# Kernel tuning notes

Measured on AMD Instinct MI355X. Metric: run time of the kernel, lower is better.

The kernel has to match this reference:

```python
import jax, jax.numpy as jnp
import numpy as np

B, S, HID = 2, 2048, 4096
NH, NKV, HD = 32, 8, 128
SCALING = HD ** -0.5
Q_SIZE = NH * HD          # 4096
KV_SIZE = NKV * HD        # 1024
GROUPS = NH // NKV        # 4


def setup_inputs() -> dict:
    key = jax.random.key(0)
    ks = jax.random.split(key, 5)
    hidden_states = jax.random.normal(ks[0], (B, S, HID), dtype=jnp.float32)
    # Realistic rotary embeddings: cos/sin of position-dependent angles, HF layout [B, S, HD]
    inv_freq = 1.0 / (10000.0 ** (jnp.arange(0, HD, 2, dtype=jnp.float32) / HD))  # [HD/2]
    pos = jnp.arange(S, dtype=jnp.float32)
    freqs = pos[:, None] * inv_freq[None, :]                 # [S, HD/2]
    emb = jnp.concatenate([freqs, freqs], axis=-1)           # [S, HD]
    cos = jnp.broadcast_to(jnp.cos(emb), (B, S, HD))
    sin = jnp.broadcast_to(jnp.sin(emb), (B, S, HD))
    w_qkv = jax.random.normal(ks[1], (Q_SIZE + 2 * KV_SIZE, HID), dtype=jnp.float32) * (HID ** -0.5)
    w_o = jax.random.normal(ks[2], (HID, Q_SIZE), dtype=jnp.float32) * (Q_SIZE ** -0.5)
    return {"hidden_states": hidden_states, "cos": cos, "sin": sin, "w_qkv": w_qkv, "w_o": w_o}


def _rotate_half(x):
    x1, x2 = jnp.split(x, 2, axis=-1)
    return jnp.concatenate([-x2, x1], axis=-1)


def reference(hidden_states, cos, sin, w_qkv, w_o):
    b, s, _ = hidden_states.shape
    # Fused QKV projection (attention_bias=False for llama)
    qkv = jnp.einsum('bsh,oh->bso', hidden_states, w_qkv)    # [B, S, Q+2KV]
    q = qkv[..., :Q_SIZE].reshape(b, s, NH, HD).transpose(0, 2, 1, 3)                       # [B, NH, S, D]
    k = qkv[..., Q_SIZE:Q_SIZE + KV_SIZE].reshape(b, s, NKV, HD).transpose(0, 2, 1, 3)      # [B, NKV, S, D]
    v = qkv[..., Q_SIZE + KV_SIZE:].reshape(b, s, NKV, HD).transpose(0, 2, 1, 3)            # [B, NKV, S, D]
    # Rotary position embedding (HF apply_rotary_pos_emb, unsqueeze over heads)
    c = cos[:, None, :, :]
    sn = sin[:, None, :, :]
    q = q * c + _rotate_half(q) * sn
    k = k * c + _rotate_half(k) * sn
    # GQA: repeat KV heads across groups
    k = jnp.repeat(k, GROUPS, axis=1)   # [B, NH, S, D]
    v = jnp.repeat(v, GROUPS, axis=1)
    # Causal SDPA
    scores = jnp.einsum('bhqd,bhkd->bhqk', q, k) * SCALING
    causal = jnp.tril(jnp.ones((s, s), dtype=bool))
    scores = jnp.where(causal[None, None], scores, jnp.finfo(scores.dtype).min)
    attn = jax.nn.softmax(scores, axis=-1)
    out = jnp.einsum('bhqk,bhkd->bhqd', attn, v)             # [B, NH, S, D]
    out = out.transpose(0, 2, 1, 3).reshape(b, s, Q_SIZE)    # [B, S, HID]
    return jnp.einsum('bso,ho->bsh', out, w_o)
```

## Files before the change

### kernel.cpp

```cpp
#include <hip/hip_runtime.h>
#include <hip/hip_bf16.h>
#include <cstdint>

#define B_DIM 2
#define S_LEN 2048
#define HID 4096
#define NH 32
#define NKV 8
#define HD 128
#define QSZ (NH * HD)
#define KVSZ (NKV * HD)
#define QKVW (QSZ + 2 * KVSZ)
#define SCALING 0.08838834764831845f

typedef __bf16 bf16;
typedef __bf16 bf16x4 __attribute__((ext_vector_type(4)));
typedef __bf16 bf16x8 __attribute__((ext_vector_type(8)));
typedef float floatx4 __attribute__((ext_vector_type(4)));

typedef __attribute__((address_space(1))) void GV;
typedef __attribute__((address_space(3))) void SV;

#define BAR() __builtin_amdgcn_s_barrier()
#define SCHED_FENCE() __builtin_amdgcn_sched_barrier(0)

__global__ __launch_bounds__(256) void cvt2(const float* __restrict__ a, bf16* __restrict__ oa, int na4,
                                            const float* __restrict__ b, bf16* __restrict__ ob, int nb4) {
    int total = na4 + nb4;
    int stride = gridDim.x * blockDim.x;
    for (int i = blockIdx.x * blockDim.x + threadIdx.x; i < total; i += stride) {
        const float* src; bf16* dst; int j = i;
        if (j < na4) { src = a; dst = oa; }
        else { j -= na4; src = b; dst = ob; }
        float4 v = ((const float4*)src)[j];
        bf16x4 o;
        o[0] = (bf16)v.x; o[1] = (bf16)v.y; o[2] = (bf16)v.z; o[3] = (bf16)v.w;
        ((bf16x4*)dst)[j] = o;
    }
}

template <int MODE, typename OutT>
__global__ __launch_bounds__(512, 2) void gemm256(const bf16* __restrict__ A,
                                                  const bf16* __restrict__ Bm,
                                                  OutT* __restrict__ C,
                                                  bf16* __restrict__ Qo,
                                                  bf16* __restrict__ Ko,
                                                  bf16* __restrict__ Vo,
                                                  const float* __restrict__ cosp,
                                                  const float* __restrict__ sinp,
                                                  const float* __restrict__ cvt_src,
                                                  bf16* __restrict__ cvt_dst,
                                                  int cvt_n4, int ngemm,
                                                  int M, int N, int K) {
    __shared__ __align__(16) char smem[131072];
    (void)M;
    int bid = blockIdx.x;
    int tid = threadIdx.x;
    if (bid >= ngemm) {
        int stride = (gridDim.x - ngemm) * 512;
        for (int i = (bid - ngemm) * 512 + tid; i < cvt_n4; i += stride) {
            float4 v = ((const float4*)cvt_src)[i];
            bf16x4 o;
            o[0] = (bf16)v.x; o[1] = (bf16)v.y; o[2] = (bf16)v.z; o[3] = (bf16)v.w;
            ((bf16x4*)cvt_dst)[i] = o;
        }
        return;
    }
    int tiles_n = N >> 8;
    int wg = (bid & 7) * (ngemm >> 3) + (bid >> 3);
    int bm = wg / tiles_n, bn = wg % tiles_n;
    int lane = tid & 63, w = tid >> 6;
    int l15 = lane & 15, lg = lane >> 4, l7 = l15 & 7;
    int wm = w >> 2, wn = w & 3;
    const bf16* Ab = A + (size_t)bm * 256 * K;
    const bf16* Bb = Bm + (size_t)bn * 256 * K;

    auto AsP = [&](int buf, int h) -> char* { return smem + (buf * 2 + h) * 16384; };
    auto BsP = [&](int buf, int h) -> char* { return smem + 65536 + (buf * 2 + h) * 16384; };

    int o_lo = tid * 16, o_hi = o_lo + 8192;
    int r_lo = o_lo >> 7, r_hi = o_hi >> 7;
    int eo0 = r_lo * K + ((((o_lo >> 4) & 7) ^ (r_lo & 7)) << 3);
    int eo1 = r_hi * K + ((((o_hi >> 4) & 7) ^ (r_hi & 7)) << 3);
    const bf16* AbH[2] = {Ab, Ab + (size_t)128 * K};
    const bf16* BbH[2] = {Bb, Bb + (size_t)128 * K};

    auto stageA = [&](int buf, int h, int kt) {
        const bf16* base = AbH[h] + kt * 64;
        __builtin_amdgcn_global_load_lds((GV*)(base + eo0), (SV*)(AsP(buf, h) + o_lo), 16, 0, 0);
        __builtin_amdgcn_global_load_lds((GV*)(base + eo1), (SV*)(AsP(buf, h) + o_hi), 16, 0, 0);
    };
    auto stageB = [&](int buf, int h, int kt) {
        const bf16* base = BbH[h] + kt * 64;
        __builtin_amdgcn_global_load_lds((GV*)(base + eo0), (SV*)(BsP(buf, h) + o_lo), 16, 0, 0);
        __builtin_amdgcn_global_load_lds((GV*)(base + eo1), (SV*)(BsP(buf, h) + o_hi), 16, 0, 0);
    };
    auto rdA = [&](int buf, int fr, int kk) -> bf16x8 {
        int off = (fr * 16 + l15) * 128 + ((((kk << 2) | lg) ^ l7) << 4);
        return *(const bf16x8*)(AsP(buf, wm) + off);
    };
    auto rdB = [&](int buf, int fc, int kk) -> bf16x8 {
        int off = ((wn & 1) * 64 + fc * 16 + l15) * 128 + ((((kk << 2) | lg) ^ l7) << 4);
        return *(const bf16x8*)(BsP(buf, wn >> 1) + off);
    };

    floatx4 acc[8][4] = {};
    bf16x8 aF[4][2], bF[4][2];
    int nk = K >> 6, niter = nk >> 1;

    stageA(0, 0, 0); stageA(0, 1, 0); stageB(0, 0, 0); stageB(0, 1, 0);
    stageB(1, 0, 1); stageB(1, 1, 1);
    asm volatile("s_waitcnt vmcnt(4)" ::: "memory");
    SCHED_FENCE();
    BAR();

    auto quad = [&](int ra, int ca) {
        __builtin_amdgcn_s_setprio(1);
#pragma unroll
        for (int fr = 0; fr < 4; ++fr)
#pragma unroll
            for (int fc = 0; fc < 2; ++fc)
#pragma unroll
                for (int kk = 0; kk < 2; ++kk)
                    acc[ra * 4 + fr][ca * 2 + fc] = __builtin_amdgcn_mfma_f32_16x16x32_bf16(
                        aF[fr][kk], bF[ca * 2 + fc][kk], acc[ra * 4 + fr][ca * 2 + fc], 0, 0, 0);
        __builtin_amdgcn_s_setprio(0);
    };

    for (int i = 0; i < niter; ++i) {
        bool nl = (i + 1 < niter);
        int kt1 = 2 * i + 1, kt2 = 2 * i + 2, kt3 = 2 * i + 3;
#pragma unroll
        for (int fr = 0; fr < 4; ++fr)
#pragma unroll
            for (int kk = 0; kk < 2; ++kk) aF[fr][kk] = rdA(0, fr, kk);
#pragma unroll
        for (int fc = 0; fc < 2; ++fc)
#pragma unroll
            for (int kk = 0; kk < 2; ++kk) bF[fc][kk] = rdB(0, fc, kk);
        stageA(1, 0, kt1);
        BAR(); quad(0, 0); BAR();
#pragma unroll
        for (int fc = 2; fc < 4; ++fc)
#pragma unroll
            for (int kk = 0; kk < 2; ++kk) bF[fc][kk] = rdB(0, fc, kk);
        stageA(1, 1, kt1);
        BAR(); quad(0, 1); BAR();
#pragma unroll
        for (int fr = 0; fr < 4; ++fr)
#pragma unroll
            for (int kk = 0; kk < 2; ++kk) aF[fr][kk] = rdA(0, 4 + fr, kk);
        if (nl) stageB(0, 0, kt2);
        BAR(); quad(1, 0); BAR();
        if (nl) stageB(0, 1, kt2);
        BAR(); quad(1, 1);
        if (nl) asm volatile("s_waitcnt vmcnt(4)" ::: "memory");
        else    asm volatile("s_waitcnt vmcnt(0)" ::: "memory");
        SCHED_FENCE();
        BAR();
#pragma unroll
        for (int fr = 0; fr < 4; ++fr)
#pragma unroll
            for (int kk = 0; kk < 2; ++kk) aF[fr][kk] = rdA(1, fr, kk);
#pragma unroll
        for (int fc = 0; fc < 2; ++fc)
#pragma unroll
            for (int kk = 0; kk < 2; ++kk) bF[fc][kk] = rdB(1, fc, kk);
        if (nl) stageA(0, 0, kt2);
        BAR(); quad(0, 0); BAR();
#pragma unroll
        for (int fc = 2; fc < 4; ++fc)
#pragma unroll
            for (int kk = 0; kk < 2; ++kk) bF[fc][kk] = rdB(1, fc, kk);
        if (nl) stageA(0, 1, kt2);
        BAR(); quad(0, 1); BAR();
#pragma unroll
        for (int fr = 0; fr < 4; ++fr)
#pragma unroll
            for (int kk = 0; kk < 2; ++kk) aF[fr][kk] = rdA(1, 4 + fr, kk);
        if (nl) stageB(1, 0, kt3);
        BAR(); quad(1, 0); BAR();
        if (nl) stageB(1, 1, kt3);
        BAR(); quad(1, 1);
        asm volatile("s_waitcnt vmcnt(4)" ::: "memory");
        SCHED_FENCE();
        BAR();
    }

    if constexpr (MODE == 0) {
        int brow = bm * 256 + wm * 128, bcol = bn * 256 + wn * 64;
#pragma unroll
        for (int fr = 0; fr < 8; ++fr)
#pragma unroll
            for (int fc = 0; fc < 4; ++fc) {
                int col = bcol + fc * 16 + l15;
#pragma unroll
                for (int r = 0; r < 4; ++r) {
                    int row = brow + fr * 16 + lg * 4 + r;
                    C[(size_t)row * N + col] = (OutT)acc[fr][fc][r];
                }
            }
    } else {
        __syncthreads();
        int b = (bm * 256) >> 11, s0 = (bm * 256) & (S_LEN - 1);
        int colb = wn * 64, rowb = wm * 128;
        if (bn < 20) {
            bf16* Cb = (bf16*)smem;
#pragma unroll
            for (int fr = 0; fr < 8; ++fr)
#pragma unroll
                for (int fc = 0; fc < 4; ++fc) {
                    int col = colb + fc * 16 + l15;
                    int br = rowb + fr * 16 + lg * 4;
#pragma unroll
                    for (int r = 0; r < 4; ++r) {
                        int row = br + r;
                        Cb[row * 256 + ((((col >> 3) ^ (row & 7)) << 3) | (col & 7))] =
                            (bf16)acc[fr][fc][r];
                    }
                }
            __syncthreads();
            bool isQ = (bn < 16);
            int hh = w & 1;
            int c = l15, d0 = c * 8;
            float scale = isQ ? SCALING : 1.0f;
            float sgn = (c < 8) ? -1.0f : 1.0f;
            bf16* Ob = isQ ? (Qo + ((size_t)(b * NH + bn * 2 + hh) * S_LEN) * HD)
                           : (Ko + ((size_t)(b * NKV + (bn - 16) * 2 + hh) * S_LEN) * HD);
            int slot_s = hh * 16 + c, slot_p = hh * 16 + (c ^ 8);
#pragma unroll
            for (int rd = 0; rd < 16; ++rd) {
                int row = (w >> 1) * 64 + rd * 4 + lg;
                int s = s0 + row;
                bf16x8 xs = *(const bf16x8*)(Cb + row * 256 + ((slot_s ^ (row & 7)) << 3));
                bf16x8 xp = *(const bf16x8*)(Cb + row * 256 + ((slot_p ^ (row & 7)) << 3));
                const float* cr = cosp + ((size_t)b * S_LEN + s) * HD + d0;
                const float* sr = sinp + ((size_t)b * S_LEN + s) * HD + d0;
                float4 c0 = *(const float4*)cr, c1 = *(const float4*)(cr + 4);
                float4 s0v = *(const float4*)sr, s1v = *(const float4*)(sr + 4);
                float cv[8] = {c0.x, c0.y, c0.z, c0.w, c1.x, c1.y, c1.z, c1.w};
                float sv[8] = {s0v.x, s0v.y, s0v.z, s0v.w, s1v.x, s1v.y, s1v.z, s1v.w};
                bf16x8 o;
#pragma unroll
                for (int e = 0; e < 8; ++e)
                    o[e] = (bf16)(((float)xs[e] * cv[e] + sgn * (float)xp[e] * sv[e]) * scale);
                *(bf16x8*)(Ob + (size_t)s * HD + d0) = o;
            }
        } else {
#pragma unroll
            for (int fr = 0; fr < 8; ++fr)
#pragma unroll
                for (int fc = 0; fc < 4; ++fc) {
                    int col = colb + fc * 16 + l15;
                    int br = rowb + fr * 16 + lg * 4;
#pragma unroll
                    for (int r = 0; r < 4; ++r) {
                        int row = br + r;
                        *(bf16*)(smem + col * 512 +
                                 (((((row >> 3) ^ (col & 7)) << 4) | ((row & 7) << 1)))) =
                            (bf16)acc[fr][fc][r];
                    }
                }
            __syncthreads();
            int kvb = (bn - 20) * 2;
            int sc = tid & 31;
            int dgr = tid >> 5;
#pragma unroll
            for (int j = 0; j < 16; ++j) {
                int col = dgr * 16 + j;
                int kv = kvb + (col >> 7), d = col & 127;
                bf16x8 o = *(const bf16x8*)(smem + col * 512 + ((sc ^ (col & 7)) << 4));
                *(bf16x8*)(Vo + ((size_t)(b * NKV + kv) * HD + d) * S_LEN + s0 + sc * 8) = o;
            }
        }
    }
}

__global__ __launch_bounds__(256, 2) void attn_fwd(const bf16* __restrict__ Q,
                                                   const bf16* __restrict__ K,
                                                   const bf16* __restrict__ Vt,
                                                   bf16* __restrict__ O) {
    __shared__ __align__(16) bf16 Ks[2][64 * 128];
    __shared__ __align__(16) bf16 Vs[2][128 * 64];
    __shared__ __align__(16) bf16 Ps[4][32 * 64];

    int ord = blockIdx.x;
    int qt = 15 - (ord >> 6);
    int bh = ord & 63;
    int h = bh & 31, b = bh >> 5;
    int kvh = h >> 2;
    int tid = threadIdx.x, lane = tid & 63, w = tid >> 6;
    int l15 = lane & 15, lg = lane >> 4, l7 = l15 & 7, lg4 = lg * 4;
    int q0 = qt * 128;
    int qbw = q0 + w * 32;

    const bf16* Qb = Q + ((size_t)(b * NH + h) * S_LEN) * HD;
    const bf16* Kb = K + ((size_t)(b * NKV + kvh) * S_LEN) * HD;
    const bf16* Vb = Vt + ((size_t)(b * NKV + kvh) * HD) * S_LEN;

    bf16x8 qf[2][4];
#pragma unroll
    for (int i = 0; i < 2; ++i)
#pragma unroll
        for (int ks = 0; ks < 4; ++ks)
            qf[i][ks] = *(const bf16x8*)(Qb + (size_t)(qbw + i * 16 + l15) * HD + ks * 32 + lg * 8);

    floatx4 accO[2][8] = {};
    float m_run[2] = {-1e30f, -1e30f}, l_run[2] = {0.f, 0.f};

    char* Pc = (char*)Ps[w];
    int nt = 2 * qt + 2;

    auto stageK = [&](int buf, int t) {
        int kv0 = t * 64;
#pragma unroll
        for (int it = 0; it < 4; ++it) {
            int o = it * 4096 + tid * 16;
            int r = o >> 8, pb = (o >> 4) & 15;
            int lb = pb ^ (r & 7);
            __builtin_amdgcn_global_load_lds((GV*)(Kb + (size_t)(kv0 + r) * HD + lb * 8),
                                             (SV*)((char*)Ks[buf] + o), 16, 0, 0);
        }
    };
    auto stageV = [&](int buf, int t) {
        int kv0 = t * 64;
#pragma unroll
        for (int it = 0; it < 4; ++it) {
            int o = it * 4096 + tid * 16;
            int d = o >> 7, pb = (o >> 4) & 7;
            int lb = pb ^ (d & 7);
            __builtin_amdgcn_global_load_lds((GV*)(Vb + (size_t)d * S_LEN + kv0 + lb * 8),
                                             (SV*)((char*)Vs[buf] + o), 16, 0, 0);
        }
    };

    stageK(0, 0);
    stageV(0, 0);

    for (int t = 0; t < nt; ++t) {
        int cur = t & 1;
        int kv0 = t * 64;
        bool more = (t + 1 < nt);
        if (more) { stageK(cur ^ 1, t + 1); stageV(cur ^ 1, t + 1); }
        if (more) asm volatile("s_waitcnt vmcnt(8)" ::: "memory");
        else      asm volatile("s_waitcnt vmcnt(0)" ::: "memory");
        SCHED_FENCE();
        BAR();

        const char* Kc = (const char*)Ks[cur];
        const char* Vc = (const char*)Vs[cur];
        floatx4 s[2][4] = {};
        __builtin_amdgcn_s_setprio(1);
#pragma unroll
        for (int nm = 0; nm < 4; ++nm)
#pragma unroll
            for (int ks = 0; ks < 4; ++ks) {
                bf16x8 kf = *(const bf16x8*)(Kc + (nm * 16 + l15) * 256 +
                                             ((((ks << 2) | lg) ^ l7) << 4));
                s[0][nm] = __builtin_amdgcn_mfma_f32_16x16x32_bf16(kf, qf[0][ks], s[0][nm], 0, 0, 0);
                s[1][nm] = __builtin_amdgcn_mfma_f32_16x16x32_bf16(kf, qf[1][ks], s[1][nm], 0, 0, 0);
            }
        __builtin_amdgcn_s_setprio(0);

#pragma unroll
        for (int i = 0; i < 2; ++i) {
            if (kv0 + 63 > qbw + i * 16) {
                int qg = qbw + i * 16 + l15;
#pragma unroll
                for (int nm = 0; nm < 4; ++nm)
#pragma unroll
                    for (int r = 0; r < 4; ++r)
                        if (kv0 + nm * 16 + lg4 + r > qg) s[i][nm][r] = -1e30f;
            }
            float t0 = fmaxf(fmaxf(s[i][0][0], s[i][0][1]), fmaxf(s[i][0][2], s[i][0][3]));
            float t1 = fmaxf(fmaxf(s[i][1][0], s[i][1][1]), fmaxf(s[i][1][2], s[i][1][3]));
            float t2 = fmaxf(fmaxf(s[i][2][0], s[i][2][1]), fmaxf(s[i][2][2], s[i][2][3]));
            float t3 = fmaxf(fmaxf(s[i][3][0], s[i][3][1]), fmaxf(s[i][3][2], s[i][3][3]));
            float pm = fmaxf(fmaxf(t0, t1), fmaxf(t2, t3));
            pm = fmaxf(pm, __shfl_xor(pm, 16));
            pm = fmaxf(pm, __shfl_xor(pm, 32));
            bool need = !__all(pm - m_run[i] <= 8.f);
            float corr = 1.f;
            if (need) {
                float mn = fmaxf(m_run[i], pm);
                corr = __expf(m_run[i] - mn);
                m_run[i] = mn;
            }
            float mn = m_run[i];
            float sum = 0.f;
#pragma unroll
            for (int nm = 0; nm < 4; ++nm) {
                bf16x4 pk;
#pragma unroll
                for (int r = 0; r < 4; ++r) {
                    float p = __expf(s[i][nm][r] - mn);
                    sum += p;
                    pk[r] = (bf16)p;
                }
                *(bf16x4*)(Pc + (i * 16 + l15) * 128 +
                           ((((nm << 1) | (lg >> 1)) ^ l7) << 4) + ((lg & 1) << 3)) = pk;
            }
            sum += __shfl_xor(sum, 16);
            sum += __shfl_xor(sum, 32);
            if (need) {
                l_run[i] = l_run[i] * corr + sum;
#pragma unroll
                for (int r = 0; r < 4; ++r) {
                    float cr = __shfl(corr, lg4 + r);
#pragma unroll
                    for (int g = 0; g < 8; ++g) accO[i][g][r] *= cr;
                }
            } else {
                l_run[i] += sum;
            }
        }

        asm volatile("s_waitcnt lgkmcnt(0)" ::: "memory");
        SCHED_FENCE();

        bf16x8 pf[2][2];
#pragma unroll
        for (int i = 0; i < 2; ++i)
#pragma unroll
            for (int ks = 0; ks < 2; ++ks)
                pf[i][ks] = *(const bf16x8*)(Pc + (i * 16 + l15) * 128 +
                                             ((((ks << 2) | lg) ^ l7) << 4));
        __builtin_amdgcn_s_setprio(1);
#pragma unroll
        for (int g = 0; g < 8; ++g)
#pragma unroll
            for (int ks = 0; ks < 2; ++ks) {
                bf16x8 vf = *(const bf16x8*)(Vc + (g * 16 + l15) * 128 +
                                             ((((ks << 2) | lg) ^ l7) << 4));
                accO[0][g] = __builtin_amdgcn_mfma_f32_16x16x32_bf16(pf[0][ks], vf, accO[0][g], 0, 0, 0);
                accO[1][g] = __builtin_amdgcn_mfma_f32_16x16x32_bf16(pf[1][ks], vf, accO[1][g], 0, 0, 0);
            }
        __builtin_amdgcn_s_setprio(0);
        BAR();
    }

#pragma unroll
    for (int i = 0; i < 2; ++i) {
        float inv = 1.f / l_run[i];
#pragma unroll
        for (int r = 0; r < 4; ++r) {
            float vinv = __shfl(inv, lg4 + r);
            int qg = qbw + i * 16 + lg4 + r;
            size_t ob = ((size_t)(b * S_LEN + qg) * NH + h) * HD;
#pragma unroll
            for (int g = 0; g < 8; ++g)
                O[ob + g * 16 + l15] = (bf16)(accO[i][g][r] * vinv);
        }
    }
}

extern "C" void kernel_launch(void* const* d_in, const int* in_sizes, int n_in,
                              void* d_out, int out_size, void* d_ws, size_t ws_size,
                              hipStream_t stream) {
    const float* hs   = (const float*)d_in[0];
    const float* cosp = (const float*)d_in[1];
    const float* sinp = (const float*)d_in[2];
    const float* wqkv = (const float*)d_in[3];
    const float* wo   = (const float*)d_in[4];
    float* out = (float*)d_out;

    char* ws = (char*)d_ws;
    size_t off = 0;
    auto alloc = [&](size_t bytes) {
        char* p = ws + off;
        off += (bytes + 255) & ~(size_t)255;
        return p;
    };
    const size_t n_hs = (size_t)B_DIM * S_LEN * HID;
    const size_t n_wqkv = (size_t)QKVW * HID;
    const size_t n_wo = (size_t)HID * QSZ;

    bf16* hs_b   = (bf16*)alloc(n_hs * 2);
    bf16* wqkv_b = (bf16*)alloc(n_wqkv * 2);
    bf16* wo_b   = (bf16*)alloc(n_wo * 2);
    bf16* Qb  = (bf16*)alloc((size_t)B_DIM * NH * S_LEN * HD * 2);
    bf16* Kb  = (bf16*)alloc((size_t)B_DIM * NKV * S_LEN * HD * 2);
    bf16* Vtb = (bf16*)alloc((size_t)B_DIM * NKV * HD * S_LEN * 2);
    bf16* attn_b = hs_b;

    cvt2<<<1536, 256, 0, stream>>>(hs, hs_b, (int)(n_hs >> 2),
                                   wqkv, wqkv_b, (int)(n_wqkv >> 2));

    const int ngemm1 = (4096 / 256) * (6144 / 256);
    gemm256<1, bf16><<<ngemm1 + 64, 512, 0, stream>>>(
        hs_b, wqkv_b, (bf16*)nullptr, Qb, Kb, Vtb, cosp, sinp,
        wo, wo_b, (int)(n_wo >> 2), ngemm1, B_DIM * S_LEN, QKVW, HID);

    attn_fwd<<<B_DIM * NH * (S_LEN / 128), 256, 0, stream>>>(Qb, Kb, Vtb, attn_b);

    gemm256<0, float><<<(4096 / 256) * (4096 / 256), 512, 0, stream>>>(
        attn_b, wo_b, out, nullptr, nullptr, nullptr, nullptr, nullptr,
        nullptr, nullptr, 0, (4096 / 256) * (4096 / 256),
        B_DIM * S_LEN, HID, HID);
}
```

Baseline: 469.6 us.

## Triple-buffer B tiles and prefetch next-tile fragments in the GEMM main loop

```diff
diff --git a/kernel.cpp b/kernel.cpp
--- a/kernel.cpp
+++ b/kernel.cpp
@@ -52,7 +52,7 @@
                                                   bf16* __restrict__ cvt_dst,
                                                   int cvt_n4, int ngemm,
                                                   int M, int N, int K) {
-    __shared__ __align__(16) char smem[131072];
+    __shared__ __align__(16) char smem[163840];
     (void)M;
     int bid = blockIdx.x;
     int tid = threadIdx.x;
@@ -75,8 +75,8 @@
     const bf16* Ab = A + (size_t)bm * 256 * K;
     const bf16* Bb = Bm + (size_t)bn * 256 * K;
 
-    auto AsP = [&](int buf, int h) -> char* { return smem + (buf * 2 + h) * 16384; };
-    auto BsP = [&](int buf, int h) -> char* { return smem + 65536 + (buf * 2 + h) * 16384; };
+    auto AsP = [&](int buf) -> char* { return smem + buf * 32768; };
+    auto BsP = [&](int buf) -> char* { return smem + 65536 + buf * 32768; };
 
     int o_lo = tid * 16, o_hi = o_lo + 8192;
     int r_lo = o_lo >> 7, r_hi = o_hi >> 7;
@@ -87,105 +87,110 @@
 
     auto stageA = [&](int buf, int h, int kt) {
         const bf16* base = AbH[h] + kt * 64;
-        __builtin_amdgcn_global_load_lds((GV*)(base + eo0), (SV*)(AsP(buf, h) + o_lo), 16, 0, 0);
-        __builtin_amdgcn_global_load_lds((GV*)(base + eo1), (SV*)(AsP(buf, h) + o_hi), 16, 0, 0);
+        char* d = AsP(buf) + h * 16384;
+        __builtin_amdgcn_global_load_lds((GV*)(base + eo0), (SV*)(d + o_lo), 16, 0, 0);
+        __builtin_amdgcn_global_load_lds((GV*)(base + eo1), (SV*)(d + o_hi), 16, 0, 0);
     };
     auto stageB = [&](int buf, int h, int kt) {
         const bf16* base = BbH[h] + kt * 64;
-        __builtin_amdgcn_global_load_lds((GV*)(base + eo0), (SV*)(BsP(buf, h) + o_lo), 16, 0, 0);
-        __builtin_amdgcn_global_load_lds((GV*)(base + eo1), (SV*)(BsP(buf, h) + o_hi), 16, 0, 0);
+        char* d = BsP(buf) + h * 16384;
+        __builtin_amdgcn_global_load_lds((GV*)(base + eo0), (SV*)(d + o_lo), 16, 0, 0);
+        __builtin_amdgcn_global_load_lds((GV*)(base + eo1), (SV*)(d + o_hi), 16, 0, 0);
     };
     auto rdA = [&](int buf, int fr, int kk) -> bf16x8 {
-        int off = (fr * 16 + l15) * 128 + ((((kk << 2) | lg) ^ l7) << 4);
-        return *(const bf16x8*)(AsP(buf, wm) + off);
+        int off = wm * 16384 + (fr * 16 + l15) * 128 + ((((kk << 2) | lg) ^ l7) << 4);
+        return *(const bf16x8*)(AsP(buf) + off);
     };
     auto rdB = [&](int buf, int fc, int kk) -> bf16x8 {
-        int off = ((wn & 1) * 64 + fc * 16 + l15) * 128 + ((((kk << 2) | lg) ^ l7) << 4);
-        return *(const bf16x8*)(BsP(buf, wn >> 1) + off);
+        int off = (wn >> 1) * 16384 + ((wn & 1) * 64 + fc * 16 + l15) * 128 +
+                  ((((kk << 2) | lg) ^ l7) << 4);
+        return *(const bf16x8*)(BsP(buf) + off);
     };
 
     floatx4 acc[8][4] = {};
-    bf16x8 aF[4][2], bF[4][2];
-    int nk = K >> 6, niter = nk >> 1;
-
-    stageA(0, 0, 0); stageA(0, 1, 0); stageB(0, 0, 0); stageB(0, 1, 0);
+    bf16x8 a03[4][2], a47[4][2], b01A[2][2], b01B[2][2], b23[2][2];
+    const int nk = K >> 6;
+
+#define QUADM(ASET, BSET, RA, CA)                                                      \
+    __builtin_amdgcn_s_setprio(1);                                                     \
+    _Pragma("unroll") for (int fr = 0; fr < 4; ++fr)                                   \
+        _Pragma("unroll") for (int fc = 0; fc < 2; ++fc)                               \
+            _Pragma("unroll") for (int kk = 0; kk < 2; ++kk)                           \
+                acc[(RA)*4 + fr][(CA)*2 + fc] = __builtin_amdgcn_mfma_f32_16x16x32_bf16( \
+                    ASET[fr][kk], BSET[fc][kk], acc[(RA)*4 + fr][(CA)*2 + fc], 0, 0, 0); \
+    __builtin_amdgcn_s_setprio(0);
+
+#define TILE(T, AP, AN, BCUR, BNXT, BSTG, B01C, B01N)                                  \
+    {                                                                                  \
+        bool st = (T) + 2 < nk;                                                        \
+        bool nx = (T) + 1 < nk;                                                        \
+                                                                               \
+        _Pragma("unroll") for (int fc = 0; fc < 2; ++fc)                               \
+            _Pragma("unroll") for (int kk = 0; kk < 2; ++kk)                           \
+                b23[fc][kk] = rdB(BCUR, 2 + fc, kk);                                   \
+        if (st) stageB(BSTG, 0, (T) + 2);                                              \
+        BAR();                                                                         \
+        QUADM(a03, B01C, 0, 0);                                                        \
+        BAR();                                                                         \
+                                                                               \
+        _Pragma("unroll") for (int fr = 0; fr < 4; ++fr)                               \
+            _Pragma("unroll") for (int kk = 0; kk < 2; ++kk)                           \
+                a47[fr][kk] = rdA(AP, 4 + fr, kk);                                     \
+        if (st) stageB(BSTG, 1, (T) + 2);                                              \
+        BAR();                                                                         \
+        QUADM(a03, b23, 0, 1);                                                         \
+        if (st) asm volatile("s_waitcnt vmcnt(4)" ::: "memory");                       \
+        else    asm volatile("s_waitcnt vmcnt(0)" ::: "memory");                       \
+        SCHED_FENCE();                                                                 \
+        BAR();                                                                         \
+                                                                               \
+        if (nx) {                                                                      \
+            _Pragma("unroll") for (int fr = 0; fr < 4; ++fr)                           \
+                _Pragma("unroll") for (int kk = 0; kk < 2; ++kk)                       \
+                    a03[fr][kk] = rdA(AN, fr, kk);                                     \
+            _Pragma("unroll") for (int fc = 0; fc < 2; ++fc)                           \
+                _Pragma("unroll") for (int kk = 0; kk < 2; ++kk)                       \
+                    B01N[fc][kk] = rdB(BNXT, fc, kk);                                  \
+        }                                                                              \
+        if (st) stageA(AP, 0, (T) + 2);                                                \
+        BAR();                                                                         \
+        QUADM(a47, B01C, 1, 0);                                                        \
+        BAR();                                                                         \
+                                                                               \
+        if (st) stageA(AP, 1, (T) + 2);                                                \
+        BAR();                                                                         \
+        QUADM(a47, b23, 1, 1);                                                         \
+        BAR();                                                                         \
+    }
+
+    stageA(0, 0, 0); stageA(0, 1, 0);
+    stageB(0, 0, 0); stageB(0, 1, 0);
+    stageA(1, 0, 1); stageA(1, 1, 1);
     stageB(1, 0, 1); stageB(1, 1, 1);
-    asm volatile("s_waitcnt vmcnt(4)" ::: "memory");
+    asm volatile("s_waitcnt vmcnt(8)" ::: "memory");
     SCHED_FENCE();
     BAR();
-
-    auto quad = [&](int ra, int ca) {
-        __builtin_amdgcn_s_setprio(1);
-#pragma unroll
-        for (int fr = 0; fr < 4; ++fr)
-#pragma unroll
-            for (int fc = 0; fc < 2; ++fc)
-#pragma unroll
-                for (int kk = 0; kk < 2; ++kk)
-                    acc[ra * 4 + fr][ca * 2 + fc] = __builtin_amdgcn_mfma_f32_16x16x32_bf16(
-                        aF[fr][kk], bF[ca * 2 + fc][kk], acc[ra * 4 + fr][ca * 2 + fc], 0, 0, 0);
-        __builtin_amdgcn_s_setprio(0);
-    };
-
-    for (int i = 0; i < niter; ++i) {
-        bool nl = (i + 1 < niter);
-        int kt1 = 2 * i + 1, kt2 = 2 * i + 2, kt3 = 2 * i + 3;
-#pragma unroll
-        for (int fr = 0; fr < 4; ++fr)
-#pragma unroll
-            for (int kk = 0; kk < 2; ++kk) aF[fr][kk] = rdA(0, fr, kk);
-#pragma unroll
-        for (int fc = 0; fc < 2; ++fc)
-#pragma unroll
-            for (int kk = 0; kk < 2; ++kk) bF[fc][kk] = rdB(0, fc, kk);
-        stageA(1, 0, kt1);
-        BAR(); quad(0, 0); BAR();
-#pragma unroll
-        for (int fc = 2; fc < 4; ++fc)
-#pragma unroll
-            for (int kk = 0; kk < 2; ++kk) bF[fc][kk] = rdB(0, fc, kk);
-        stageA(1, 1, kt1);
-        BAR(); quad(0, 1); BAR();
-#pragma unroll
-        for (int fr = 0; fr < 4; ++fr)
-#pragma unroll
-            for (int kk = 0; kk < 2; ++kk) aF[fr][kk] = rdA(0, 4 + fr, kk);
-        if (nl) stageB(0, 0, kt2);
-        BAR(); quad(1, 0); BAR();
-        if (nl) stageB(0, 1, kt2);
-        BAR(); quad(1, 1);
-        if (nl) asm volatile("s_waitcnt vmcnt(4)" ::: "memory");
-        else    asm volatile("s_waitcnt vmcnt(0)" ::: "memory");
-        SCHED_FENCE();
-        BAR();
-#pragma unroll
-        for (int fr = 0; fr < 4; ++fr)
-#pragma unroll
-            for (int kk = 0; kk < 2; ++kk) aF[fr][kk] = rdA(1, fr, kk);
-#pragma unroll
-        for (int fc = 0; fc < 2; ++fc)
-#pragma unroll
-            for (int kk = 0; kk < 2; ++kk) bF[fc][kk] = rdB(1, fc, kk);
-        if (nl) stageA(0, 0, kt2);
-        BAR(); quad(0, 0); BAR();
-#pragma unroll
-        for (int fc = 2; fc < 4; ++fc)
-#pragma unroll
-            for (int kk = 0; kk < 2; ++kk) bF[fc][kk] = rdB(1, fc, kk);
-        if (nl) stageA(0, 1, kt2);
-        BAR(); quad(0, 1); BAR();
-#pragma unroll
-        for (int fr = 0; fr < 4; ++fr)
-#pragma unroll
-            for (int kk = 0; kk < 2; ++kk) aF[fr][kk] = rdA(1, 4 + fr, kk);
-        if (nl) stageB(1, 0, kt3);
-        BAR(); quad(1, 0); BAR();
-        if (nl) stageB(1, 1, kt3);
-        BAR(); quad(1, 1);
-        asm volatile("s_waitcnt vmcnt(4)" ::: "memory");
-        SCHED_FENCE();
-        BAR();
-    }
+#pragma unroll
+    for (int fr = 0; fr < 4; ++fr)
+#pragma unroll
+        for (int kk = 0; kk < 2; ++kk) a03[fr][kk] = rdA(0, fr, kk);
+#pragma unroll
+    for (int fc = 0; fc < 2; ++fc)
+#pragma unroll
+        for (int kk = 0; kk < 2; ++kk) b01A[fc][kk] = rdB(0, fc, kk);
+
+    int bb = 0;
+    for (int i = 0; i < (nk >> 1); ++i) {
+        int t0 = 2 * i;
+        int b0 = bb;
+        int b1 = b0 + 1; if (b1 >= 3) b1 -= 3;
+        int b2 = b1 + 1; if (b2 >= 3) b2 -= 3;
+        TILE(t0, 0, 1, b0, b1, b2, b01A, b01B);
+        TILE(t0 + 1, 1, 0, b1, b2, b0, b01B, b01A);
+        bb = b2;
+    }
+#undef TILE
+#undef QUADM
 
     if constexpr (MODE == 0) {
         int brow = bm * 256 + wm * 128, bcol = bn * 256 + wn * 64;
```

Result: slower. 1.167 ms (+148.5%).
